# Kernel optimization log

Hardware: AMD Instinct MI355X
Metric: run time of the kernel (lower is better)

Reference implementation:

```python
import jax, jax.numpy as jnp
import numpy as np

BATCH, QLEN, KVLEN = 4, 8, 512
C, H = 512, 8
N = C // H  # 64
D_W, D_A, D_V, D_G = 32, 32, 32, 96
GN_EPS = 1e-5 * 8 ** 2  # head_size_divisor = 8


def setup_inputs() -> dict:
    key = jax.random.key(0)
    ks = jax.random.split(key, 32)
    rn = lambda i, sh, s=1.0: jax.random.normal(ks[i], sh, dtype=jnp.float32) * s
    ru = lambda i, sh: jax.random.uniform(ks[i], sh, dtype=jnp.float32)
    s = C ** -0.5
    return {
        "query": rn(0, (BATCH, QLEN, C)),
        "keyval": rn(1, (BATCH, KVLEN, C)),
        "v_first": rn(2, (BATCH * QLEN, KVLEN, C)),
        "x_r": ru(3, (1, 1, C)), "x_w": ru(4, (1, 1, C)), "x_k": ru(5, (1, 1, C)),
        "x_v": ru(6, (1, 1, C)), "x_a": ru(7, (1, 1, C)), "x_g": ru(8, (1, 1, C)),
        "w0": jnp.linspace(-7.0, -2.0, C, dtype=jnp.float32).reshape(1, 1, C) + 0.5,
        "w1": rn(9, (C, D_W), 0.02), "w2": rn(10, (D_W, C), 0.02),
        "a0": rn(11, (1, 1, C), 0.01), "a1": rn(12, (C, D_A), 0.02), "a2": rn(13, (D_A, C), 0.02),
        "v0": jnp.ones((1, 1, C), jnp.float32), "v1": rn(14, (C, D_V), 0.02), "v2": rn(15, (D_V, C), 0.02),
        "g1": rn(16, (C, D_G), 0.02), "g2": rn(17, (D_G, C), 0.02),
        "k_k": 0.85 + rn(18, (1, 1, C), 0.02), "k_a": jnp.ones((1, 1, C), jnp.float32),
        "r_k": rn(19, (H, N), 0.02),
        "Wr": rn(20, (C, C), 0.5 * s), "Wk": rn(21, (C, C), 0.05 * s),
        "Wv": rn(22, (C, C), 0.5 * s), "Wo": rn(23, (C, C), s),
        "ln_w": 1.0 + rn(24, (C,), 0.02), "ln_b": rn(25, (C,), 0.02),
    }


def _rwkv7_scan(r, w, k, v, a, b):
    # r,w,k,v,a,b: [B,T,C]; RWKV7 generalized delta rule, state [B,H,N,N] (value x key).
    B, T, _ = r.shape
    toTBHN = lambda t: t.reshape(B, T, H, N).transpose(1, 0, 2, 3)  # [T,B,H,N]
    rT, kT, vT, aT, bT = map(toTBHN, (r, k, v, a, b))
    wT = jnp.exp(-jnp.exp(toTBHN(w)))  # decay in (0,1)

    def step(state, xs):
        r_t, w_t, k_t, v_t, a_t, b_t = xs
        sa = jnp.einsum('bhij,bhj->bhi', state, a_t)  # state @ a
        state = (state * w_t[:, :, None, :]
                 + sa[..., None] * b_t[:, :, None, :]
                 + v_t[..., None] * k_t[:, :, None, :])
        out = jnp.einsum('bhij,bhj->bhi', state, r_t)
        return state, out

    state0 = jnp.zeros((B, H, N, N), dtype=jnp.float32)
    _, outs = jax.lax.scan(step, state0, (rT, wT, kT, vT, aT, bT))
    return outs.transpose(1, 0, 2, 3).reshape(B, T, C)  # [B,T,C]


def _forward(query, keyval, v_first, x_r, x_w, x_k, x_v, x_a, x_g,
             w0, w1, w2, a0, a1, a2, v0, v1, v2, g1, g2,
             k_k, k_a, r_k, Wr, Wk, Wv, Wo, ln_w, ln_b):
    batch, qlen, Cc = query.shape
    kvlen = keyval.shape[1]
    # cross-product expansion: every (query token, keyval sequence) pair
    eq = jnp.repeat(query[:, :, None, :], kvlen, axis=2).reshape(-1, kvlen, Cc)
    ek = jnp.repeat(keyval[:, None, :, :], qlen, axis=1).reshape(-1, kvlen, Cc)
    B, T = ek.shape[0], kvlen
    xx_cross = eq - ek
    shifted = jnp.pad(ek, ((0, 0), (1, 0), (0, 0)))[:, :-1]  # time_shift
    xx_kv = shifted - ek
    x = ek
    xr = x + xx_cross * x_r
    xw = x + xx_cross * x_w
    xa = x + xx_cross * x_a
    xg = x + xx_cross * x_g
    xk = x + xx_kv * x_k
    xv = x + xx_kv * x_v

    r = xr @ Wr
    w = -jax.nn.softplus(-(w0 + jnp.tanh(xw @ w1) @ w2)) - 0.5
    k = xk @ Wk
    v = xv @ Wv
    v = v + (v_first - v) * jax.nn.sigmoid(v0 + (xv @ v1) @ v2)  # layer_id != 0
    a = jax.nn.sigmoid(a0 + (xa @ a1) @ a2)
    g = jax.nn.sigmoid(xg @ g1) @ g2

    kk = k * k_k
    kkh = kk.reshape(B, T, H, N)
    kkh = kkh / jnp.maximum(jnp.linalg.norm(kkh, axis=-1, keepdims=True), 1e-12)
    kk = kkh.reshape(B, T, Cc)
    k = k * (1.0 + (a - 1.0) * k_a)

    xo = _rwkv7_scan(r, w, k, v, -kk, kk * a)

    # GroupNorm over H groups of N channels, eps = 1e-5 * head_size_divisor^2
    y = xo.reshape(B * T, H, N)
    mu = y.mean(axis=-1, keepdims=True)
    var = y.var(axis=-1, keepdims=True)
    yn = (y - mu) * jax.lax.rsqrt(var + GN_EPS)
    xo = (yn.reshape(B * T, Cc) * ln_w + ln_b).reshape(B, T, Cc)

    rk = (r.reshape(B, T, H, N) * k.reshape(B, T, H, N) * r_k).sum(axis=-1, keepdims=True)
    xo = xo + (rk * v.reshape(B, T, H, N)).reshape(B, T, Cc)
    xo = xo * g
    xo = xo[:, -1, :]  # frames=None path
    xo = xo.reshape(batch, qlen, Cc) @ Wo
    return xo, v_first


def reference(query, keyval, v_first, x_r, x_w, x_k, x_v, x_a, x_g,
              w0, w1, w2, a0, a1, a2, v0, v1, v2, g1, g2,
              k_k, k_a, r_k, Wr, Wk, Wv, Wo, ln_w, ln_b):
    return _forward(query, keyval, v_first, x_r, x_w, x_k, x_v, x_a, x_g,
                    w0, w1, w2, a0, a1, a2, v0, v1, v2, g1, g2,
                    k_k, k_a, r_k, Wr, Wk, Wv, Wo, ln_w, ln_b)
```

## Files before the change

kernel.cpp:

```cpp
#include <hip/hip_runtime.h>
#include <cstdint>

#define TT 512
#define CC 512
#define HH 8
#define NN 64
#define BQ 32
#define NB 4

__device__ __forceinline__ float sigm(float x){ return 1.f/(1.f+__expf(-x)); }

__device__ __forceinline__ float wsum(float x){
  #pragma unroll
  for (int o=32;o;o>>=1) x += __shfl_xor(x, o, 64);
  return x;
}

template<int NR>
__device__ __forceinline__ void rowsum64_batch(float* x){
  #pragma unroll
  for (int i=0;i<NR;i++)
    x[i] += __int_as_float(__builtin_amdgcn_mov_dpp(__float_as_int(x[i]), 0x121, 0xf, 0xf, true));
  #pragma unroll
  for (int i=0;i<NR;i++)
    x[i] += __int_as_float(__builtin_amdgcn_mov_dpp(__float_as_int(x[i]), 0x122, 0xf, 0xf, true));
  #pragma unroll
  for (int i=0;i<NR;i++)
    x[i] += __int_as_float(__builtin_amdgcn_mov_dpp(__float_as_int(x[i]), 0x124, 0xf, 0xf, true));
  #pragma unroll
  for (int i=0;i<NR;i++)
    x[i] += __int_as_float(__builtin_amdgcn_mov_dpp(__float_as_int(x[i]), 0x128, 0xf, 0xf, true));
  float y[NR];
  #pragma unroll
  for (int i=0;i<NR;i++) asm("v_mov_b32 %0, %1" : "=v"(y[i]) : "v"(x[i]));
  #pragma unroll
  for (int i=0;i<NR;i++) asm("v_permlane16_swap_b32 %0, %1" : "+v"(x[i]), "+v"(y[i]));
  #pragma unroll
  for (int i=0;i<NR;i++) x[i] += y[i];
  #pragma unroll
  for (int i=0;i<NR;i++) asm("v_mov_b32 %0, %1" : "=v"(y[i]) : "v"(x[i]));
  #pragma unroll
  for (int i=0;i<NR;i++) asm("v_permlane32_swap_b32 %0, %1" : "+v"(x[i]), "+v"(y[i]));
  #pragma unroll
  for (int i=0;i<NR;i++) x[i] += y[i];
}

__global__ __launch_bounds__(256) void k_prep(
  const float* __restrict__ q, const float* __restrict__ kv,
  const float* __restrict__ x_r, const float* __restrict__ x_w,
  const float* __restrict__ x_a, const float* __restrict__ x_g,
  const float* __restrict__ w1, const float* __restrict__ a1,
  const float* __restrict__ g1,
  float* __restrict__ Qw, float* __restrict__ Qa,
  float* __restrict__ ghw, float* __restrict__ xrw)
{
  int bq = blockIdx.x, b = bq >> 3, tid = threadIdx.x;
  int wave = tid >> 6, lane = tid & 63;
  __shared__ float qxw[CC], qxa[CC], sxg[CC];
  for (int c = tid; c < CC; c += 256){
    float qv = q[bq*CC + c];
    float kl = kv[((size_t)b*TT + (TT-1))*CC + c];
    xrw[bq*CC + c] = kl + (qv - kl)*x_r[c];
    sxg[c] = kl + (qv - kl)*x_g[c];
    qxw[c] = qv*x_w[c];
    qxa[c] = qv*x_a[c];
  }
  __syncthreads();
  for (int dot = wave; dot < 160; dot += 4){
    const float* buf; const float* W; int ld, dd;
    if (dot < 32)      { buf = qxw; W = w1; ld = 32; dd = dot; }
    else if (dot < 64) { buf = qxa; W = a1; ld = 32; dd = dot-32; }
    else               { buf = sxg; W = g1; ld = 96; dd = dot-64; }
    float s = 0.f;
    #pragma unroll
    for (int m = 0; m < 8; m++){
      int c = m*64 + lane;
      s = fmaf(buf[c], W[c*ld + dd], s);
    }
    s = wsum(s);
    if (lane == 0){
      if (dot < 32)      Qw[bq*32 + dd] = s;
      else if (dot < 64) Qa[bq*32 + dd] = s;
      else               ghw[bq*96 + dd] = sigm(s);
    }
  }
}

__global__ __launch_bounds__(256) void k_rg(
  const float* __restrict__ xrw, const float* __restrict__ ghw,
  const float* __restrict__ Wr, const float* __restrict__ g2,
  float* __restrict__ rrow, float* __restrict__ grow)
{
  int bq = blockIdx.y; int co0 = blockIdx.x*64;
  int tid = threadIdx.x, tx = tid & 63, ty = tid >> 6;
  __shared__ float sxr[CC];
  __shared__ float sgh[96];
  __shared__ float red[4][64];
  sxr[tid]     = xrw[bq*CC + tid];
  sxr[tid+256] = xrw[bq*CC + tid + 256];
  if (tid < 96) sgh[tid] = ghw[bq*96 + tid];
  __syncthreads();
  float p = 0.f;
  for (int i = 0; i < 128; i++){
    int c = ty*128 + i;
    p = fmaf(sxr[c], Wr[(size_t)c*CC + co0 + tx], p);
  }
  red[ty][tx] = p;
  float pg = 0.f;
  for (int d = ty*24; d < ty*24 + 24; d++)
    pg = fmaf(sgh[d], g2[(size_t)d*CC + co0 + tx], pg);
  __syncthreads();
  if (ty == 0)
    rrow[bq*CC + co0 + tx] = (red[0][tx]+red[1][tx])+(red[2][tx]+red[3][tx]);
  __syncthreads();
  red[ty][tx] = pg;
  __syncthreads();
  if (ty == 0)
    grow[bq*CC + co0 + tx] = (red[0][tx]+red[1][tx])+(red[2][tx]+red[3][tx]);
}

__global__ __launch_bounds__(256) void k_shift(
  const float* __restrict__ kv, const float* __restrict__ x_k,
  const float* __restrict__ x_v,
  float* __restrict__ xk, float* __restrict__ xv)
{
  int g = blockIdx.x*256 + threadIdx.x;
  int bt = g >> 7, t = bt & (TT-1), c4 = g & 127;
  const float4* kv4 = (const float4*)kv;
  float4 cur = kv4[g];
  float4 sh  = t ? kv4[g-128] : make_float4(0.f,0.f,0.f,0.f);
  float4 kc  = ((const float4*)x_k)[c4];
  float4 vc  = ((const float4*)x_v)[c4];
  float4 ok, ov;
  ok.x = cur.x + (sh.x-cur.x)*kc.x; ov.x = cur.x + (sh.x-cur.x)*vc.x;
  ok.y = cur.y + (sh.y-cur.y)*kc.y; ov.y = cur.y + (sh.y-cur.y)*vc.y;
  ok.z = cur.z + (sh.z-cur.z)*kc.z; ov.z = cur.z + (sh.z-cur.z)*vc.z;
  ok.w = cur.w + (sh.w-cur.w)*kc.w; ov.w = cur.w + (sh.w-cur.w)*vc.w;
  ((float4*)xk)[g] = ok;
  ((float4*)xv)[g] = ov;
}

__global__ __launch_bounds__(256) void k_pgemm(
  const float* __restrict__ kv, const float* __restrict__ xv,
  const float* __restrict__ x_w, const float* __restrict__ x_a,
  const float* __restrict__ w1, const float* __restrict__ a1,
  const float* __restrict__ v1,
  float* __restrict__ Pw, float* __restrict__ Pa, float* __restrict__ HV)
{
  int mat = blockIdx.y;
  int r0 = blockIdx.x * 64;
  const float* A = (mat == 2) ? xv : kv;
  const float* B = (mat == 0) ? w1 : (mat == 1) ? a1 : v1;
  float* O       = (mat == 0) ? Pw : (mat == 1) ? Pa : HV;
  int tid = threadIdx.x;
  __shared__ float As[32][65];
  __shared__ float Bs[32][32];
  __shared__ float scl[CC];
  for (int c = tid; c < CC; c += 256)
    scl[c] = (mat == 0) ? (1.f - x_w[c]) : (mat == 1) ? (1.f - x_a[c]) : 1.f;
  __syncthreads();
  int tx = tid & 31, ty = tid >> 5;
  float acc[8];
  #pragma unroll
  for (int i = 0; i < 8; i++) acc[i] = 0.f;
  for (int k0 = 0; k0 < 512; k0 += 32){
    #pragma unroll
    for (int p = 0; p < 8; p++){
      int e = tid + p*256;
      int kk2 = e & 31, r = e >> 5;
      As[kk2][r] = A[(size_t)(r0+r)*512 + k0 + kk2] * scl[k0 + kk2];
    }
    #pragma unroll
    for (int p = 0; p < 4; p++){
      int e = tid + p*256;
      int n = e & 31, kk2 = e >> 5;
      Bs[kk2][n] = B[(size_t)(k0+kk2)*32 + n];
    }
    __syncthreads();
    #pragma unroll
    for (int kk2 = 0; kk2 < 32; kk2++){
      float bb = Bs[kk2][tx];
      #pragma unroll
      for (int i = 0; i < 8; i++)
        acc[i] = fmaf(As[kk2][ty*8 + i], bb, acc[i]);
    }
    __syncthreads();
  }
  #pragma unroll
  for (int i = 0; i < 8; i++)
    O[(size_t)(r0 + ty*8 + i)*32 + tx] = acc[i];
}

__global__ __launch_bounds__(256) void k_sv(
  const float* __restrict__ HV, const float* __restrict__ v2,
  const float* __restrict__ v0, float* __restrict__ svv)
{
  int bt = blockIdx.x, tid = threadIdx.x;
  __shared__ float hv[32];
  if (tid < 32) hv[tid] = HV[bt*32 + tid];
  __syncthreads();
  for (int c = tid; c < CC; c += 256){
    float s = 0.f;
    #pragma unroll
    for (int d = 0; d < 32; d++) s = fmaf(hv[d], v2[d*CC + c], s);
    svv[(size_t)bt*CC + c] = sigm(v0[c] + s);
  }
}

__global__ __launch_bounds__(256) void gemm_2048_512(
  const float* __restrict__ A, const float* __restrict__ W, float* __restrict__ Co)
{
  __shared__ float As[32][68];
  __shared__ float Bs[32][64];
  int tid = threadIdx.x;
  int tx = tid & 15, ty = tid >> 4;
  int m0 = blockIdx.y*64, n0 = blockIdx.x*64;
  float acc[4][4];
  #pragma unroll
  for (int i=0;i<4;i++)
    #pragma unroll
    for (int j=0;j<4;j++) acc[i][j]=0.f;

  for (int k0 = 0; k0 < 512; k0 += 32){
    #pragma unroll
    for (int i = 0; i < 8; i++){
      int e = tid + i*256;
      int kk = e & 31, m = e >> 5;
      As[kk][m] = A[(size_t)(m0+m)*512 + k0 + kk];
    }
    #pragma unroll
    for (int i = 0; i < 8; i++){
      int e = tid + i*256;
      int n = e & 63, kk = e >> 6;
      Bs[kk][n] = W[(size_t)(k0+kk)*512 + n0 + n];
    }
    __syncthreads();
    #pragma unroll
    for (int kk = 0; kk < 32; kk++){
      float a4[4], b4[4];
      #pragma unroll
      for (int i=0;i<4;i++) a4[i] = As[kk][ty*4+i];
      #pragma unroll
      for (int j=0;j<4;j++) b4[j] = Bs[kk][tx*4+j];
      #pragma unroll
      for (int i=0;i<4;i++)
        #pragma unroll
        for (int j=0;j<4;j++) acc[i][j] += a4[i]*b4[j];
    }
    __syncthreads();
  }
  #pragma unroll
  for (int i=0;i<4;i++)
    #pragma unroll
    for (int j=0;j<4;j++)
      Co[(size_t)(m0+ty*4+i)*512 + n0 + tx*4 + j] = acc[i][j];
}

__global__ __launch_bounds__(512) void k_kk(
  const float* __restrict__ kg, const float* __restrict__ k_k,
  float* __restrict__ kkg)
{
  int bt = blockIdx.x, tid = threadIdx.x;
  float v = kg[(size_t)bt*CC + tid]*k_k[tid];
  float ss = wsum(v*v);
  float nrm = fmaxf(sqrtf(ss), 1e-12f);
  kkg[(size_t)bt*CC + tid] = v/nrm;
}

__global__ __launch_bounds__(256) void k_wkb(
  const float* __restrict__ Pw, const float* __restrict__ Pa,
  const float* __restrict__ Qw, const float* __restrict__ Qa,
  const float* __restrict__ w2, const float* __restrict__ a2,
  const float* __restrict__ w0, const float* __restrict__ a0,
  const float* __restrict__ k_a, const float* __restrict__ kg,
  const float* __restrict__ kkg,
  float* __restrict__ wS, float* __restrict__ kS, float* __restrict__ bS)
{
  int bqt0 = blockIdx.x*4;
  int bq = bqt0 >> 9, t0 = bqt0 & (TT-1), b = bq >> 3;
  int tid = threadIdx.x;
  __shared__ float sth[4][32], sal[4][32];
  {
    int g = (tid >> 5) & 3, d = tid & 31;
    int pidx = ((b << 9) | (t0 + g))*32 + d;
    if (tid < 128) sth[g][d] = tanhf(Pw[pidx] + Qw[bq*32 + d]);
    else           sal[g][d] = Pa[pidx] + Qa[bq*32 + d];
  }
  __syncthreads();
  #pragma unroll
  for (int cc = 0; cc < 2; cc++){
    int c = tid + cc*256;
    float wreg[32], areg[32];
    #pragma unroll
    for (int d = 0; d < 32; d++){ wreg[d] = w2[d*CC + c]; areg[d] = a2[d*CC + c]; }
    float w0c = w0[c], a0c = a0[c], kac = k_a[c];
    #pragma unroll
    for (int g = 0; g < 4; g++){
      float wa = 0.f, aa = 0.f;
      #pragma unroll
      for (int d = 0; d < 32; d++){
        wa = fmaf(sth[g][d], wreg[d], wa);
        aa = fmaf(sal[g][d], areg[d], aa);
      }
      float a_sig = sigm(a0c + aa);
      float wdec  = __expf(-0.60653066f * sigm(w0c + wa));
      size_t bt = (size_t)((b << 9) | (t0 + g));
      size_t o  = (size_t)(bqt0 + g)*CC + c;
      float kvv = kg[bt*CC + c];
      float kkv = kkg[bt*CC + c];
      wS[o] = wdec;
      kS[o] = kvv*(1.f + (a_sig - 1.f)*kac);
      bS[o] = kkv*a_sig;
    }
  }
}

__global__ __launch_bounds__(64) void k_scan(
  const float* __restrict__ wv, const float* __restrict__ kf,
  const float* __restrict__ bv, const float* __restrict__ kkg,
  const float* __restrict__ vpre, const float* __restrict__ svv,
  const float* __restrict__ vfirst,
  const float* __restrict__ rrow, const float* __restrict__ grow,
  const float* __restrict__ r_k, const float* __restrict__ ln_w,
  const float* __restrict__ ln_b, float* __restrict__ xo)
{
  int blk = blockIdx.x; int bq = blk >> 3, h = blk & 7, b = bq >> 3;
  int lane = threadIdx.x & 63;
  size_t cb_bq = (size_t)bq*TT*CC + h*NN;
  size_t cb_b  = (size_t)b*TT*CC + h*NN;

  const float* pw  = wv     + cb_bq + lane;
  const float* pk  = kf     + cb_bq + lane;
  const float* pb  = bv     + cb_bq + lane;
  const float* pa  = kkg    + cb_b  + lane;
  const float* pvp = vpre   + cb_b  + lane;
  const float* psv = svv    + cb_b  + lane;
  const float* pvf = vfirst + cb_bq + lane;

  float g   = rrow[(size_t)bq*CC + h*NN + lane];
  float out = 0.f;

  constexpr int D = 8;
  float fw[D], fk[D], fb[D], fa[D], fp[D], fs[D], fv[D];
  #pragma unroll
  for (int d = 0; d < D; ++d){
    size_t o = (size_t)(TT-1-d)*CC;
    fw[d]=pw[o]; fk[d]=pk[o]; fb[d]=pb[o]; fa[d]=pa[o];
    fp[d]=pvp[o]; fs[d]=psv[o]; fv[d]=pvf[o];
  }

  #pragma unroll 1
  for (int ob = 0; ob < TT/D; ++ob){
    int sbase = TT-1 - ob*D;
    #pragma unroll
    for (int d = 0; d < D; ++d){
      int s = sbase - d;
      float wj=fw[d], kj=fk[d], bj=fb[d], aj=fa[d];
      float vj = fp[d] + (fv[d]-fp[d])*fs[d];
      int sp = s - D; sp = sp < 0 ? 0 : sp;
      size_t o = (size_t)sp*CC;
      fw[d]=pw[o]; fk[d]=pk[o]; fb[d]=pb[o]; fa[d]=pa[o];
      fp[d]=pvp[o]; fs[d]=psv[o]; fv[d]=pvf[o];
      float red[2];
      red[0] = kj*g;
      red[1] = bj*g;
      rowsum64_batch<2>(red);
      out = fmaf(red[0], vj, out);
      g   = fmaf(wj, g, -(aj*red[1]));
    }
  }

  {
    float mean = wsum(out) * (1.f/NN);
    float dv = out - mean;
    float var = wsum(dv*dv) * (1.f/NN);
    float yn = dv * rsqrtf(var + 6.4e-4f);
    int c = h*NN + lane;
    float y2 = yn * ln_w[c] + ln_b[c];
    size_t oT = (size_t)(TT-1)*CC;
    float kl = pk[oT];
    float rl = rrow[(size_t)bq*CC + c];
    float rk = wsum(rl*kl*r_k[c]);
    float vp_ = pvp[oT], sv_ = psv[oT], vf_ = pvf[oT];
    float v_i = vp_ + (vf_ - vp_)*sv_;
    float res = (y2 + rk*v_i) * grow[(size_t)bq*CC + c];
    xo[bq*CC + c] = res;
  }
}

__global__ __launch_bounds__(256) void k_out(
  const float* __restrict__ xo, const float* __restrict__ Wo,
  float* __restrict__ outp)
{
  int bq = blockIdx.y; int co0 = blockIdx.x*64;
  int tid = threadIdx.x, tx = tid & 63, ty = tid >> 6;
  __shared__ float row[CC];
  __shared__ float red[4][64];
  row[tid]     = xo[bq*CC + tid];
  row[tid+256] = xo[bq*CC + tid + 256];
  __syncthreads();
  float p = 0.f;
  for (int i = 0; i < 128; i++){
    int c = ty*128 + i;
    p = fmaf(row[c], Wo[(size_t)c*CC + co0 + tx], p);
  }
  red[ty][tx] = p;
  __syncthreads();
  if (ty == 0)
    outp[bq*CC + co0 + tx] = (red[0][tx]+red[1][tx])+(red[2][tx]+red[3][tx]);
}

extern "C" void kernel_launch(void* const* d_in, const int* in_sizes, int n_in,
                              void* d_out, int out_size, void* d_ws, size_t ws_size,
                              hipStream_t stream)
{
  const float* q   = (const float*)d_in[0];
  const float* kv  = (const float*)d_in[1];
  const float* vf  = (const float*)d_in[2];
  const float* x_r = (const float*)d_in[3];
  const float* x_w = (const float*)d_in[4];
  const float* x_k = (const float*)d_in[5];
  const float* x_v = (const float*)d_in[6];
  const float* x_a = (const float*)d_in[7];
  const float* x_g = (const float*)d_in[8];
  const float* w0  = (const float*)d_in[9];
  const float* w1  = (const float*)d_in[10];
  const float* w2  = (const float*)d_in[11];
  const float* a0  = (const float*)d_in[12];
  const float* a1  = (const float*)d_in[13];
  const float* a2  = (const float*)d_in[14];
  const float* v0  = (const float*)d_in[15];
  const float* v1  = (const float*)d_in[16];
  const float* v2  = (const float*)d_in[17];
  const float* g1  = (const float*)d_in[18];
  const float* g2  = (const float*)d_in[19];
  const float* k_k = (const float*)d_in[20];
  const float* k_a = (const float*)d_in[21];
  const float* r_k = (const float*)d_in[22];
  const float* Wr  = (const float*)d_in[23];
  const float* Wk  = (const float*)d_in[24];
  const float* Wv  = (const float*)d_in[25];
  const float* Wo  = (const float*)d_in[26];
  const float* lnw = (const float*)d_in[27];
  const float* lnb = (const float*)d_in[28];
  float* outp = (float*)d_out;
  float* ws = (float*)d_ws;

  float* xk = ws + 0;
  float* xv = ws + 1048576;
  float* kg = ws + 2097152;
  float* vp = ws + 3145728;
  float* sv = ws + 4194304;
  float* kk = ws + 5242880;
  float* Pw = ws + 6291456;
  float* Pa = ws + 6356992;
  float* Qw = ws + 6422528;
  float* Qa = ws + 6423552;
  float* HV = ws + 6424576;
  float* rr = ws + 7473152;
  float* gr = ws + 7489536;
  float* xo = ws + 7505920;
  float* wS = ws + 7522304;
  float* kS = ws + 15910912;
  float* bS = ws + 24299520;
  float* xrw = ws + 32688128;
  float* ghw = ws + 32704512;

  hipMemcpyAsync(outp + BQ*CC, vf,
                 (size_t)BQ*TT*CC*sizeof(float), hipMemcpyDeviceToDevice, stream);

  k_prep<<<32, 256, 0, stream>>>(q, kv, x_r, x_w, x_a, x_g, w1, a1, g1,
                                 Qw, Qa, ghw, xrw);
  k_rg<<<dim3(8, 32), 256, 0, stream>>>(xrw, ghw, Wr, g2, rr, gr);
  k_shift<<<1024, 256, 0, stream>>>(kv, x_k, x_v, xk, xv);
  gemm_2048_512<<<dim3(8, 32), 256, 0, stream>>>(xk, Wk, kg);
  gemm_2048_512<<<dim3(8, 32), 256, 0, stream>>>(xv, Wv, vp);
  k_pgemm<<<dim3(32, 3), 256, 0, stream>>>(kv, xv, x_w, x_a, w1, a1, v1,
                                           Pw, Pa, HV);
  k_sv<<<NB*TT, 256, 0, stream>>>(HV, v2, v0, sv);
  k_kk<<<NB*TT, 512, 0, stream>>>(kg, k_k, kk);
  k_wkb<<<BQ*TT/4, 256, 0, stream>>>(Pw, Pa, Qw, Qa, w2, a2, w0, a0, k_a,
                                     kg, kk, wS, kS, bS);
  k_scan<<<BQ*HH, 64, 0, stream>>>(wS, kS, bS, kk, vp, sv, vf, rr, gr, r_k,
                                   lnw, lnb, xo);
  k_out<<<dim3(8, 32), 256, 0, stream>>>(xo, Wo, outp);
}
```

Baseline: 408.2 us.

## Pack scan inputs into per-head time-grouped float4 layout and merge K/V GEMMs

Producer kernels (the V GEMM, k_wkb and a new k_svpack) now write w, k, b, kk, v_pre and sv in a [b,h,tgroup,lane] float4 layout. Each scan lane can then fetch four timesteps with one 16-byte load instead of strided scalar loads spread across 2KB rows. The K and V GEMMs are merged into one launch using grid z, and the sv computation is fused with packing kk. The scan's unrolled step is restructured around a scheduling barrier, and the xk buffer is reused as scratch for kkP. The latency-bound serial scan should see fewer outstanding memory transactions, in exchange for more complex indexing and uncoalesced-looking writes in the producers.

Measured after the change: 460.0 us. 1.13x slower.

```diff
diff --git a/kernel.cpp b/kernel.cpp
--- a/kernel.cpp
+++ b/kernel.cpp
@@ -7,6 +7,7 @@
 #define NN 64
 #define BQ 32
 #define NB 4
+#define TG 128
 
 __device__ __forceinline__ float sigm(float x){ return 1.f/(1.f+__expf(-x)); }
 
@@ -191,27 +192,52 @@
     O[(size_t)(r0 + ty*8 + i)*32 + tx] = acc[i];
 }
 
-__global__ __launch_bounds__(256) void k_sv(
+__global__ __launch_bounds__(256) void k_svpack(
   const float* __restrict__ HV, const float* __restrict__ v2,
-  const float* __restrict__ v0, float* __restrict__ svv)
-{
-  int bt = blockIdx.x, tid = threadIdx.x;
-  __shared__ float hv[32];
-  if (tid < 32) hv[tid] = HV[bt*32 + tid];
-  __syncthreads();
-  for (int c = tid; c < CC; c += 256){
-    float s = 0.f;
-    #pragma unroll
-    for (int d = 0; d < 32; d++) s = fmaf(hv[d], v2[d*CC + c], s);
-    svv[(size_t)bt*CC + c] = sigm(v0[c] + s);
-  }
-}
-
-__global__ __launch_bounds__(256) void gemm_2048_512(
-  const float* __restrict__ A, const float* __restrict__ W, float* __restrict__ Co)
+  const float* __restrict__ v0, const float* __restrict__ kkg,
+  float* __restrict__ svP, float* __restrict__ kkP)
+{
+  int blk = blockIdx.x;
+  int b = blk >> 7, tg = blk & (TG-1);
+  int tid = threadIdx.x;
+  __shared__ float hv[4][32];
+  if (tid < 128){
+    int u = tid >> 5, d = tid & 31;
+    hv[u][d] = HV[((size_t)(b*TT + tg*4 + u))*32 + d];
+  }
+  __syncthreads();
+  #pragma unroll
+  for (int cc = 0; cc < 2; cc++){
+    int c = tid + cc*256;
+    int h = c >> 6, cc0 = c & 63;
+    float vcol[32];
+    #pragma unroll
+    for (int d = 0; d < 32; d++) vcol[d] = v2[d*CC + c];
+    float v0c = v0[c];
+    float sres[4], kres[4];
+    #pragma unroll
+    for (int u = 0; u < 4; u++){
+      float s = 0.f;
+      #pragma unroll
+      for (int d = 0; d < 32; d++) s = fmaf(hv[u][d], vcol[d], s);
+      sres[u] = sigm(v0c + s);
+      kres[u] = kkg[((size_t)(b*TT + tg*4 + u))*CC + c];
+    }
+    size_t o = ((size_t)(b*HH + h)*TG + tg)*64 + cc0;
+    ((float4*)svP)[o] = make_float4(sres[0],sres[1],sres[2],sres[3]);
+    ((float4*)kkP)[o] = make_float4(kres[0],kres[1],kres[2],kres[3]);
+  }
+}
+
+__global__ __launch_bounds__(256) void gemm2(
+  const float* __restrict__ A0, const float* __restrict__ W0, float* __restrict__ C0,
+  const float* __restrict__ A1, const float* __restrict__ W1, float* __restrict__ vpP)
 {
   __shared__ float As[32][68];
   __shared__ float Bs[32][64];
+  int z = blockIdx.z;
+  const float* A = z ? A1 : A0;
+  const float* W = z ? W1 : W0;
   int tid = threadIdx.x;
   int tx = tid & 15, ty = tid >> 4;
   int m0 = blockIdx.y*64, n0 = blockIdx.x*64;
@@ -249,11 +275,21 @@
     }
     __syncthreads();
   }
-  #pragma unroll
-  for (int i=0;i<4;i++)
+  if (z == 0){
+    #pragma unroll
+    for (int i=0;i<4;i++)
+      #pragma unroll
+      for (int j=0;j<4;j++)
+        C0[(size_t)(m0+ty*4+i)*512 + n0 + tx*4 + j] = acc[i][j];
+  } else {
+    int m = m0 + ty*4;
+    int b = m >> 9, t = m & (TT-1), tg = t >> 2;
+    int h = n0 >> 6;
+    float4* dst = (float4*)vpP + ((size_t)(b*HH + h)*TG + tg)*64 + tx*4;
     #pragma unroll
     for (int j=0;j<4;j++)
-      Co[(size_t)(m0+ty*4+i)*512 + n0 + tx*4 + j] = acc[i][j];
+      dst[j] = make_float4(acc[0][j],acc[1][j],acc[2][j],acc[3][j]);
+  }
 }
 
 __global__ __launch_bounds__(512) void k_kk(
@@ -274,10 +310,11 @@
   const float* __restrict__ w0, const float* __restrict__ a0,
   const float* __restrict__ k_a, const float* __restrict__ kg,
   const float* __restrict__ kkg,
-  float* __restrict__ wS, float* __restrict__ kS, float* __restrict__ bS)
+  float* __restrict__ wP, float* __restrict__ kP, float* __restrict__ bP)
 {
   int bqt0 = blockIdx.x*4;
   int bq = bqt0 >> 9, t0 = bqt0 & (TT-1), b = bq >> 3;
+  int tg = t0 >> 2;
   int tid = threadIdx.x;
   __shared__ float sth[4][32], sal[4][32];
   {
@@ -290,10 +327,12 @@
   #pragma unroll
   for (int cc = 0; cc < 2; cc++){
     int c = tid + cc*256;
+    int h = c >> 6, cc0 = c & 63;
     float wreg[32], areg[32];
     #pragma unroll
     for (int d = 0; d < 32; d++){ wreg[d] = w2[d*CC + c]; areg[d] = a2[d*CC + c]; }
     float w0c = w0[c], a0c = a0[c], kac = k_a[c];
+    float w4a[4], k4a[4], b4a[4];
     #pragma unroll
     for (int g = 0; g < 4; g++){
       float wa = 0.f, aa = 0.f;
@@ -305,20 +344,30 @@
       float a_sig = sigm(a0c + aa);
       float wdec  = __expf(-0.60653066f * sigm(w0c + wa));
       size_t bt = (size_t)((b << 9) | (t0 + g));
-      size_t o  = (size_t)(bqt0 + g)*CC + c;
       float kvv = kg[bt*CC + c];
       float kkv = kkg[bt*CC + c];
-      wS[o] = wdec;
-      kS[o] = kvv*(1.f + (a_sig - 1.f)*kac);
-      bS[o] = kkv*a_sig;
-    }
-  }
-}
-
-__global__ __launch_bounds__(64) void k_scan(
-  const float* __restrict__ wv, const float* __restrict__ kf,
-  const float* __restrict__ bv, const float* __restrict__ kkg,
-  const float* __restrict__ vpre, const float* __restrict__ svv,
+      w4a[g] = wdec;
+      k4a[g] = kvv*(1.f + (a_sig - 1.f)*kac);
+      b4a[g] = kkv*a_sig;
+    }
+    size_t o = ((size_t)(bq*HH + h)*TG + tg)*64 + cc0;
+    ((float4*)wP)[o] = make_float4(w4a[0],w4a[1],w4a[2],w4a[3]);
+    ((float4*)kP)[o] = make_float4(k4a[0],k4a[1],k4a[2],k4a[3]);
+    ((float4*)bP)[o] = make_float4(b4a[0],b4a[1],b4a[2],b4a[3]);
+  }
+}
+
+#define SCAN_STEP(wc,kc,bc,ac,pc,sc,vfc) do{ \
+  float vj = fmaf((vfc)-(pc), (sc), (pc)); \
+  float rr[2]; rr[0]=(kc)*g; rr[1]=(bc)*g; \
+  rowsum64_batch<2>(rr); \
+  out = fmaf(rr[0], vj, out); \
+  g = fmaf((wc), g, -((ac)*rr[1])); }while(0)
+
+__global__ __launch_bounds__(64, 1) void k_scan(
+  const float* __restrict__ wP, const float* __restrict__ kP,
+  const float* __restrict__ bP, const float* __restrict__ kkP,
+  const float* __restrict__ vpP, const float* __restrict__ svP,
   const float* __restrict__ vfirst,
   const float* __restrict__ rrow, const float* __restrict__ grow,
   const float* __restrict__ r_k, const float* __restrict__ ln_w,
@@ -326,47 +375,47 @@
 {
   int blk = blockIdx.x; int bq = blk >> 3, h = blk & 7, b = bq >> 3;
   int lane = threadIdx.x & 63;
-  size_t cb_bq = (size_t)bq*TT*CC + h*NN;
-  size_t cb_b  = (size_t)b*TT*CC + h*NN;
-
-  const float* pw  = wv     + cb_bq + lane;
-  const float* pk  = kf     + cb_bq + lane;
-  const float* pb  = bv     + cb_bq + lane;
-  const float* pa  = kkg    + cb_b  + lane;
-  const float* pvp = vpre   + cb_b  + lane;
-  const float* psv = svv    + cb_b  + lane;
-  const float* pvf = vfirst + cb_bq + lane;
+
+  const float4* wp4 = (const float4*)wP  + ((size_t)(bq*HH + h))*TG*64 + lane;
+  const float4* kp4 = (const float4*)kP  + ((size_t)(bq*HH + h))*TG*64 + lane;
+  const float4* bp4 = (const float4*)bP  + ((size_t)(bq*HH + h))*TG*64 + lane;
+  const float4* ap4 = (const float4*)kkP + ((size_t)(b*HH + h))*TG*64 + lane;
+  const float4* pp4 = (const float4*)vpP + ((size_t)(b*HH + h))*TG*64 + lane;
+  const float4* sp4 = (const float4*)svP + ((size_t)(b*HH + h))*TG*64 + lane;
+  const float*  pvf = vfirst + (size_t)bq*TT*CC + h*NN + lane;
 
   float g   = rrow[(size_t)bq*CC + h*NN + lane];
   float out = 0.f;
 
-  constexpr int D = 8;
-  float fw[D], fk[D], fb[D], fa[D], fp[D], fs[D], fv[D];
-  #pragma unroll
-  for (int d = 0; d < D; ++d){
-    size_t o = (size_t)(TT-1-d)*CC;
-    fw[d]=pw[o]; fk[d]=pk[o]; fb[d]=pb[o]; fa[d]=pa[o];
-    fp[d]=pvp[o]; fs[d]=psv[o]; fv[d]=pvf[o];
+  constexpr int PD = 4;
+  float4 fw[PD], fk[PD], fb[PD], fa[PD], fp[PD], fs[PD];
+  float fv0[PD], fv1[PD], fv2[PD], fv3[PD];
+  #pragma unroll
+  for (int d = 0; d < PD; ++d){
+    int gg = TG-1 - d; int go = gg*64;
+    fw[d]=wp4[go]; fk[d]=kp4[go]; fb[d]=bp4[go]; fa[d]=ap4[go];
+    fp[d]=pp4[go]; fs[d]=sp4[go];
+    const float* pv = pvf + (size_t)(4*gg)*CC;
+    fv0[d]=pv[0]; fv1[d]=pv[CC]; fv2[d]=pv[2*CC]; fv3[d]=pv[3*CC];
   }
 
   #pragma unroll 1
-  for (int ob = 0; ob < TT/D; ++ob){
-    int sbase = TT-1 - ob*D;
-    #pragma unroll
-    for (int d = 0; d < D; ++d){
-      int s = sbase - d;
-      float wj=fw[d], kj=fk[d], bj=fb[d], aj=fa[d];
-      float vj = fp[d] + (fv[d]-fp[d])*fs[d];
-      int sp = s - D; sp = sp < 0 ? 0 : sp;
-      size_t o = (size_t)sp*CC;
-      fw[d]=pw[o]; fk[d]=pk[o]; fb[d]=pb[o]; fa[d]=pa[o];
-      fp[d]=pvp[o]; fs[d]=psv[o]; fv[d]=pvf[o];
-      float red[2];
-      red[0] = kj*g;
-      red[1] = bj*g;
-      rowsum64_batch<2>(red);
-      out = fmaf(red[0], vj, out);
-      g   = fmaf(wj, g, -(aj*red[1]));
+  for (int gb = 0; gb < TG; gb += PD){
+    #pragma unroll
+    for (int sl = 0; sl < PD; ++sl){
+      int gi = TG-1 - (gb + sl);
+      float4 w4=fw[sl], k4=fk[sl], b4=fb[sl], a4=fa[sl], p4=fp[sl], s4=fs[sl];
+      float v3=fv3[sl], v2_=fv2[sl], v1_=fv1[sl], v0_=fv0[sl];
+      int gp = gi - PD; gp = gp < 0 ? 0 : gp; int go = gp*64;
+      fw[sl]=wp4[go]; fk[sl]=kp4[go]; fb[sl]=bp4[go]; fa[sl]=ap4[go];
+      fp[sl]=pp4[go]; fs[sl]=sp4[go];
+      { const float* pv = pvf + (size_t)(4*gp)*CC;
+        fv0[sl]=pv[0]; fv1[sl]=pv[CC]; fv2[sl]=pv[2*CC]; fv3[sl]=pv[3*CC]; }
+      __builtin_amdgcn_sched_barrier(0);
+      SCAN_STEP(w4.w,k4.w,b4.w,a4.w,p4.w,s4.w,v3);
+      SCAN_STEP(w4.z,k4.z,b4.z,a4.z,p4.z,s4.z,v2_);
+      SCAN_STEP(w4.y,k4.y,b4.y,a4.y,p4.y,s4.y,v1_);
+      SCAN_STEP(w4.x,k4.x,b4.x,a4.x,p4.x,s4.x,v0_);
     }
   }
 
@@ -377,11 +426,12 @@
     float yn = dv * rsqrtf(var + 6.4e-4f);
     int c = h*NN + lane;
     float y2 = yn * ln_w[c] + ln_b[c];
-    size_t oT = (size_t)(TT-1)*CC;
-    float kl = pk[oT];
-    float rl = rrow[(size_t)bq*CC + c];
-    float rk = wsum(rl*kl*r_k[c]);
-    float vp_ = pvp[oT], sv_ = psv[oT], vf_ = pvf[oT];
+    int goT = (TG-1)*64;
+    float kl  = kp4[goT].w;
+    float rl  = rrow[(size_t)bq*CC + c];
+    float rk  = wsum(rl*kl*r_k[c]);
+    float vp_ = pp4[goT].w, sv_ = sp4[goT].w;
+    float vf_ = pvf[(size_t)(TT-1)*CC];
     float v_i = vp_ + (vf_ - vp_)*sv_;
     float res = (y2 + rk*v_i) * grow[(size_t)bq*CC + c];
     xo[bq*CC + c] = res;
@@ -446,25 +496,26 @@
   float* outp = (float*)d_out;
   float* ws = (float*)d_ws;
 
-  float* xk = ws + 0;
-  float* xv = ws + 1048576;
-  float* kg = ws + 2097152;
-  float* vp = ws + 3145728;
-  float* sv = ws + 4194304;
-  float* kk = ws + 5242880;
-  float* Pw = ws + 6291456;
-  float* Pa = ws + 6356992;
-  float* Qw = ws + 6422528;
-  float* Qa = ws + 6423552;
-  float* HV = ws + 6424576;
-  float* rr = ws + 7473152;
-  float* gr = ws + 7489536;
-  float* xo = ws + 7505920;
-  float* wS = ws + 7522304;
-  float* kS = ws + 15910912;
-  float* bS = ws + 24299520;
+  float* xk  = ws + 0;
+  float* xv  = ws + 1048576;
+  float* kg  = ws + 2097152;
+  float* vpP = ws + 3145728;
+  float* svP = ws + 4194304;
+  float* kkg = ws + 5242880;
+  float* Pw  = ws + 6291456;
+  float* Pa  = ws + 6356992;
+  float* Qw  = ws + 6422528;
+  float* Qa  = ws + 6423552;
+  float* HV  = ws + 6424576;
+  float* rr  = ws + 7473152;
+  float* gr  = ws + 7489536;
+  float* xo  = ws + 7505920;
+  float* wP  = ws + 7522304;
+  float* kP  = ws + 15910912;
+  float* bP  = ws + 24299520;
   float* xrw = ws + 32688128;
   float* ghw = ws + 32704512;
+  float* kkP = xk;
 
   hipMemcpyAsync(outp + BQ*CC, vf,
                  (size_t)BQ*TT*CC*sizeof(float), hipMemcpyDeviceToDevice, stream);
@@ -473,15 +524,14 @@
                                  Qw, Qa, ghw, xrw);
   k_rg<<<dim3(8, 32), 256, 0, stream>>>(xrw, ghw, Wr, g2, rr, gr);
   k_shift<<<1024, 256, 0, stream>>>(kv, x_k, x_v, xk, xv);
-  gemm_2048_512<<<dim3(8, 32), 256, 0, stream>>>(xk, Wk, kg);
-  gemm_2048_512<<<dim3(8, 32), 256, 0, stream>>>(xv, Wv, vp);
+  gemm2<<<dim3(8, 32, 2), 256, 0, stream>>>(xk, Wk, kg, xv, Wv, vpP);
   k_pgemm<<<dim3(32, 3), 256, 0, stream>>>(kv, xv, x_w, x_a, w1, a1, v1,
                                            Pw, Pa, HV);
-  k_sv<<<NB*TT, 256, 0, stream>>>(HV, v2, v0, sv);
-  k_kk<<<NB*TT, 512, 0, stream>>>(kg, k_k, kk);
+  k_kk<<<NB*TT, 512, 0, stream>>>(kg, k_k, kkg);
+  k_svpack<<<NB*TG, 256, 0, stream>>>(HV, v2, v0, kkg, svP, kkP);
   k_wkb<<<BQ*TT/4, 256, 0, stream>>>(Pw, Pa, Qw, Qa, w2, a2, w0, a0, k_a,
-                                     kg, kk, wS, kS, bS);
-  k_scan<<<BQ*HH, 64, 0, stream>>>(wS, kS, bS, kk, vp, sv, vf, rr, gr, r_k,
+                                     kg, kkg, wP, kP, bP);
+  k_scan<<<BQ*HH, 64, 0, stream>>>(wP, kP, bP, kkP, vpP, svP, vf, rr, gr, r_k,
                                    lnw, lnb, xo);
   k_out<<<dim3(8, 32), 256, 0, stream>>>(xo, Wo, outp);
 }
```
